# Kernel tuning notes

Hardware: AMD Instinct MI355X
Metric: run time of the kernel (lower is better)

Reference implementation:

```python
import jax, jax.numpy as jnp
import numpy as np

B, QS, FD = 16384, 1204, 7
N_CHUNKS, N_OFFSETS, WIN = 120, 5, 10


def setup_inputs() -> dict:
    key = jax.random.key(0)
    ks = jax.random.split(key, 10)
    s = 0.05
    return {
        "x": jax.random.normal(ks[0], (B, QS, FD), dtype=jnp.float32),
        "w_step": jax.random.normal(ks[1], (FD,), dtype=jnp.float32) * s,
        "b_step": jax.random.normal(ks[2], (), dtype=jnp.float32) * s,
        "wA": jax.random.normal(ks[3], (600, 128), dtype=jnp.float32) * s,
        "bA": jax.random.normal(ks[4], (128,), dtype=jnp.float32) * s,
        "wB": jax.random.normal(ks[5], (128, 32), dtype=jnp.float32) * s,
        "bB": jax.random.normal(ks[6], (32,), dtype=jnp.float32) * s,
        "wC": jax.random.normal(ks[7], (32, 2), dtype=jnp.float32) * s,
        "bC": jax.random.normal(ks[8], (2,), dtype=jnp.float32) * s,
    }


def reference(x, w_step, b_step, wA, bA, wB, bB, wC, bC):
    # fc_step: (b, qs, 7) -> (b, qs)
    out = jnp.einsum('bqf,f->bq', x, w_step) + b_step
    # Windowed max: starts[i, o] = o + i*10, window of size 10.
    starts = jnp.arange(N_CHUNKS)[:, None] * WIN + jnp.arange(N_OFFSETS)[None, :]  # (120, 5)
    idx = starts[..., None] + jnp.arange(WIN)  # (120, 5, 10)
    pooled = out[:, idx].max(axis=-1)  # (b, 120, 5)
    cat = pooled.reshape(x.shape[0], N_CHUNKS * N_OFFSETS)  # (b, 600)
    h = jax.nn.relu(cat @ wA + bA)
    h = jax.nn.relu(h @ wB + bB)
    return h @ wC + bC
```

## Files before the change

### kernel.cpp

```cpp
#include <hip/hip_runtime.h>

#define NB      16384
#define QS      1204
#define FD      7
#define ROWF    (QS * FD)
#define NCH     120
#define NOFF    5
#define WINSZ   10
#define CATN    600
#define H1N     128
#define H2N     32
#define OUTN    2
#define G       4
#define NTHR    256

__global__ __launch_bounds__(NTHR) void fused_struct3(
    const float* __restrict__ x,
    const float* __restrict__ w_step,
    const float* __restrict__ b_step,
    const float* __restrict__ wA,
    const float* __restrict__ bA,
    const float* __restrict__ wB,
    const float* __restrict__ bB,
    const float* __restrict__ wC,
    const float* __restrict__ bC,
    float* __restrict__ out)
{
    __shared__ __align__(16) float orow_s[G][QS];
    __shared__ __align__(16) float cat_s[G][CATN];
    __shared__ __align__(16) float h1_s[G][H1N];
    __shared__ __align__(16) float h2_s[G][H2N];

    const int t    = threadIdx.x;
    const int lane = t & 63;
    const int w    = t >> 6;
    const int b0   = blockIdx.x * G;

    const float w0 = w_step[0], w1 = w_step[1], w2 = w_step[2], w3 = w_step[3],
                w4 = w_step[4], w5 = w_step[5], w6 = w_step[6];
    const float bs = b_step[0];

    {
        const float* row = x + (size_t)(b0 + w) * ROWF;
        for (int q = lane; q < QS; q += 64) {
            const float* p = row + q * FD;
            float s = fmaf(p[0], w0, bs);
            s = fmaf(p[1], w1, s);
            s = fmaf(p[2], w2, s);
            s = fmaf(p[3], w3, s);
            s = fmaf(p[4], w4, s);
            s = fmaf(p[5], w5, s);
            s = fmaf(p[6], w6, s);
            orow_s[w][q] = s;
        }
    }
    __syncthreads();

    for (int j = t; j < G * CATN; j += NTHR) {
        int g  = j / CATN;
        int jj = j - g * CATN;
        int ci = jj / NOFF;
        int o  = jj - ci * NOFF;
        int st = ci * WINSZ + o;
        float m = orow_s[g][st];
        #pragma unroll
        for (int u = 1; u < WINSZ; ++u) m = fmaxf(m, orow_s[g][st + u]);
        cat_s[g][jj] = m;
    }
    __syncthreads();

    float4* red = (float4*)&orow_s[0][0];
    {
        const int c4 = t & 31;
        const int g  = (t >> 5) & 3;
        const int kh = t >> 7;
        const int k0 = kh * (CATN / 2);
        const float* wAp = wA + (size_t)k0 * H1N + 4 * c4;
        const float* cp  = &cat_s[g][k0];
        float4 acc = make_float4(0.f, 0.f, 0.f, 0.f);
        #pragma unroll 4
        for (int k = 0; k < CATN / 2; ++k) {
            const float4 a = *(const float4*)(wAp + (size_t)k * H1N);
            const float  c = cp[k];
            acc.x = fmaf(c, a.x, acc.x);
            acc.y = fmaf(c, a.y, acc.y);
            acc.z = fmaf(c, a.z, acc.z);
            acc.w = fmaf(c, a.w, acc.w);
        }
        red[t] = acc;
    }
    __syncthreads();
    if (t < 128) {
        const int c4 = t & 31;
        const int g  = t >> 5;
        const float4 a = red[t];
        const float4 b = red[t + 128];
        const float4 bias = *(const float4*)(bA + 4 * c4);
        h1_s[g][4 * c4 + 0] = fmaxf(a.x + b.x + bias.x, 0.f);
        h1_s[g][4 * c4 + 1] = fmaxf(a.y + b.y + bias.y, 0.f);
        h1_s[g][4 * c4 + 2] = fmaxf(a.z + b.z + bias.z, 0.f);
        h1_s[g][4 * c4 + 3] = fmaxf(a.w + b.w + bias.w, 0.f);
    }
    __syncthreads();

    if (t < G * H2N) {
        const int g = t >> 5;
        const int n = t & 31;
        float acc = bB[n];
        #pragma unroll 8
        for (int k = 0; k < H1N; ++k)
            acc = fmaf(h1_s[g][k], wB[k * H2N + n], acc);
        h2_s[g][n] = fmaxf(acc, 0.f);
    }
    __syncthreads();

    if (t < G * OUTN) {
        const int g = t >> 1;
        const int c = t & 1;
        float acc = bC[c];
        #pragma unroll
        for (int k = 0; k < H2N; ++k)
            acc = fmaf(h2_s[g][k], wC[k * OUTN + c], acc);
        out[(size_t)(b0 + g) * OUTN + c] = acc;
    }
}

extern "C" void kernel_launch(void* const* d_in, const int* in_sizes, int n_in,
                              void* d_out, int out_size, void* d_ws, size_t ws_size,
                              hipStream_t stream) {
    const float* x      = (const float*)d_in[0];
    const float* w_step = (const float*)d_in[1];
    const float* b_step = (const float*)d_in[2];
    const float* wA     = (const float*)d_in[3];
    const float* bA     = (const float*)d_in[4];
    const float* wB     = (const float*)d_in[5];
    const float* bB     = (const float*)d_in[6];
    const float* wC     = (const float*)d_in[7];
    const float* bC     = (const float*)d_in[8];
    float* out = (float*)d_out;

    dim3 grid(NB / G);
    fused_struct3<<<grid, NTHR, 0, stream>>>(
        x, w_step, b_step, wA, bA, wB, bB, wC, bC, out);
}
```

Before: 852.8 us.

## Vectorize projection loads, share window prefix maxima, reuse wA across batch rows

The step projection now loads seven float4 per lane and produces four outputs at once, with the shared row padded so these vector stores stay in bounds. Pooling computes the five offset windows of a chunk from shared suffix and prefix maxima instead of five separate 10-element scans. The first dense layer splits K into eight slices, with each thread handling all four batch rows so every wA load is reused four times. The partial sums are then reduced across slices. A launch-bounds occupancy hint is also added, which trades more registers per thread against fewer global weight reads.

```diff
diff --git a/kernel.cpp b/kernel.cpp
--- a/kernel.cpp
+++ b/kernel.cpp
@@ -2,6 +2,7 @@
 
 #define NB      16384
 #define QS      1204
+#define QSP     1216
 #define FD      7
 #define ROWF    (QS * FD)
 #define NCH     120
@@ -14,7 +15,7 @@
 #define G       4
 #define NTHR    256
 
-__global__ __launch_bounds__(NTHR) void fused_struct3(
+__global__ __launch_bounds__(NTHR, 5) void fused_struct3(
     const float* __restrict__ x,
     const float* __restrict__ w_step,
     const float* __restrict__ b_step,
@@ -26,7 +27,7 @@
     const float* __restrict__ bC,
     float* __restrict__ out)
 {
-    __shared__ __align__(16) float orow_s[G][QS];
+    __shared__ __align__(16) float orow_s[G][QSP];
     __shared__ __align__(16) float cat_s[G][CATN];
     __shared__ __align__(16) float h1_s[G][H1N];
     __shared__ __align__(16) float h2_s[G][H2N];
@@ -42,64 +43,121 @@
 
     {
         const float* row = x + (size_t)(b0 + w) * ROWF;
-        for (int q = lane; q < QS; q += 64) {
-            const float* p = row + q * FD;
-            float s = fmaf(p[0], w0, bs);
-            s = fmaf(p[1], w1, s);
-            s = fmaf(p[2], w2, s);
-            s = fmaf(p[3], w3, s);
-            s = fmaf(p[4], w4, s);
-            s = fmaf(p[5], w5, s);
-            s = fmaf(p[6], w6, s);
-            orow_s[w][q] = s;
-        }
-    }
-    __syncthreads();
-
-    for (int j = t; j < G * CATN; j += NTHR) {
-        int g  = j / CATN;
-        int jj = j - g * CATN;
-        int ci = jj / NOFF;
-        int o  = jj - ci * NOFF;
-        int st = ci * WINSZ + o;
-        float m = orow_s[g][st];
+        for (int i = 0; i < 5; ++i) {
+            const int q0 = i * 256 + 4 * lane;
+            if (q0 < QS) {
+                const float4* p = (const float4*)(row + q0 * FD);
+                const float4 v0 = p[0], v1 = p[1], v2 = p[2], v3 = p[3],
+                             v4 = p[4], v5 = p[5], v6 = p[6];
+                float s0 = bs, s1 = bs, s2 = bs, s3 = bs;
+                s0 = fmaf(v0.x, w0, s0); s0 = fmaf(v0.y, w1, s0); s0 = fmaf(v0.z, w2, s0);
+                s0 = fmaf(v0.w, w3, s0); s0 = fmaf(v1.x, w4, s0); s0 = fmaf(v1.y, w5, s0);
+                s0 = fmaf(v1.z, w6, s0);
+                s1 = fmaf(v1.w, w0, s1); s1 = fmaf(v2.x, w1, s1); s1 = fmaf(v2.y, w2, s1);
+                s1 = fmaf(v2.z, w3, s1); s1 = fmaf(v2.w, w4, s1); s1 = fmaf(v3.x, w5, s1);
+                s1 = fmaf(v3.y, w6, s1);
+                s2 = fmaf(v3.z, w0, s2); s2 = fmaf(v3.w, w1, s2); s2 = fmaf(v4.x, w2, s2);
+                s2 = fmaf(v4.y, w3, s2); s2 = fmaf(v4.z, w4, s2); s2 = fmaf(v4.w, w5, s2);
+                s2 = fmaf(v5.x, w6, s2);
+                s3 = fmaf(v5.y, w0, s3); s3 = fmaf(v5.z, w1, s3); s3 = fmaf(v5.w, w2, s3);
+                s3 = fmaf(v6.x, w3, s3); s3 = fmaf(v6.y, w4, s3); s3 = fmaf(v6.z, w5, s3);
+                s3 = fmaf(v6.w, w6, s3);
+                *(float4*)&orow_s[w][q0] = make_float4(s0, s1, s2, s3);
+            }
+        }
+    }
+    __syncthreads();
+
+    #pragma unroll
+    for (int it = 0; it < 2; ++it) {
+        const int item = t + it * NTHR;
+        if (item < G * NCH) {
+            const int g  = item / NCH;
+            const int ci = item - g * NCH;
+            const float* v = &orow_s[g][ci * WINSZ];
+            const float4 a = *(const float4*)(v + 0);
+            const float4 b = *(const float4*)(v + 4);
+            const float4 c = *(const float4*)(v + 8);
+            const float4 d = *(const float4*)(v + 12);
+            float s9 = b.w + c.x - c.x;
+            s9 = c.y;
+            float s8 = fmaxf(c.x, s9);
+            float s7 = fmaxf(b.w, s8);
+            float s6 = fmaxf(b.z, s7);
+            float s5 = fmaxf(b.y, s6);
+            float s4 = fmaxf(b.x, s5);
+            float s3 = fmaxf(a.w, s4);
+            float s2 = fmaxf(a.z, s3);
+            float s1 = fmaxf(a.y, s2);
+            float s0 = fmaxf(a.x, s1);
+            const float p10 = c.z;
+            const float p11 = fmaxf(p10, c.w);
+            const float p12 = fmaxf(p11, d.x);
+            const float p13 = fmaxf(p12, d.y);
+            float* cp = &cat_s[g][ci * NOFF];
+            cp[0] = s0;
+            cp[1] = fmaxf(s1, p10);
+            cp[2] = fmaxf(s2, p11);
+            cp[3] = fmaxf(s3, p12);
+            cp[4] = fmaxf(s4, p13);
+        }
+    }
+    __syncthreads();
+
+    float4* red4 = (float4*)&orow_s[0][0];
+    {
+        const int c4  = t & 31;
+        const int kh  = t >> 5;
+        const int k0  = kh * 76;
+        const int len = (kh == 7) ? 68 : 76;
+        const float* wAp = wA + (size_t)k0 * H1N + 4 * c4;
+        float4 acc0 = make_float4(0.f, 0.f, 0.f, 0.f);
+        float4 acc1 = acc0, acc2 = acc0, acc3 = acc0;
+        for (int kb = 0; kb < len; kb += 4) {
+            const float4 c0 = *(const float4*)&cat_s[0][k0 + kb];
+            const float4 c1 = *(const float4*)&cat_s[1][k0 + kb];
+            const float4 c2 = *(const float4*)&cat_s[2][k0 + kb];
+            const float4 c3 = *(const float4*)&cat_s[3][k0 + kb];
+            #pragma unroll
+            for (int r = 0; r < 4; ++r) {
+                const float4 a = *(const float4*)(wAp + (size_t)(kb + r) * H1N);
+                const float e0 = (r == 0) ? c0.x : (r == 1) ? c0.y : (r == 2) ? c0.z : c0.w;
+                const float e1 = (r == 0) ? c1.x : (r == 1) ? c1.y : (r == 2) ? c1.z : c1.w;
+                const float e2 = (r == 0) ? c2.x : (r == 1) ? c2.y : (r == 2) ? c2.z : c2.w;
+                const float e3 = (r == 0) ? c3.x : (r == 1) ? c3.y : (r == 2) ? c3.z : c3.w;
+                acc0.x = fmaf(e0, a.x, acc0.x); acc0.y = fmaf(e0, a.y, acc0.y);
+                acc0.z = fmaf(e0, a.z, acc0.z); acc0.w = fmaf(e0, a.w, acc0.w);
+                acc1.x = fmaf(e1, a.x, acc1.x); acc1.y = fmaf(e1, a.y, acc1.y);
+                acc1.z = fmaf(e1, a.z, acc1.z); acc1.w = fmaf(e1, a.w, acc1.w);
+                acc2.x = fmaf(e2, a.x, acc2.x); acc2.y = fmaf(e2, a.y, acc2.y);
+                acc2.z = fmaf(e2, a.z, acc2.z); acc2.w = fmaf(e2, a.w, acc2.w);
+                acc3.x = fmaf(e3, a.x, acc3.x); acc3.y = fmaf(e3, a.y, acc3.y);
+                acc3.z = fmaf(e3, a.z, acc3.z); acc3.w = fmaf(e3, a.w, acc3.w);
+            }
+        }
+        const int base = (kh * 32 + c4) * 4;
+        red4[base + 0] = acc0;
+        red4[base + 1] = acc1;
+        red4[base + 2] = acc2;
+        red4[base + 3] = acc3;
+    }
+    __syncthreads();
+    if (t < 128) {
+        const int c4r = t >> 2;
+        const int g   = t & 3;
+        float4 s = red4[(0 * 32 + c4r) * 4 + g];
         #pragma unroll
-        for (int u = 1; u < WINSZ; ++u) m = fmaxf(m, orow_s[g][st + u]);
-        cat_s[g][jj] = m;
-    }
-    __syncthreads();
-
-    float4* red = (float4*)&orow_s[0][0];
-    {
-        const int c4 = t & 31;
-        const int g  = (t >> 5) & 3;
-        const int kh = t >> 7;
-        const int k0 = kh * (CATN / 2);
-        const float* wAp = wA + (size_t)k0 * H1N + 4 * c4;
-        const float* cp  = &cat_s[g][k0];
-        float4 acc = make_float4(0.f, 0.f, 0.f, 0.f);
-        #pragma unroll 4
-        for (int k = 0; k < CATN / 2; ++k) {
-            const float4 a = *(const float4*)(wAp + (size_t)k * H1N);
-            const float  c = cp[k];
-            acc.x = fmaf(c, a.x, acc.x);
-            acc.y = fmaf(c, a.y, acc.y);
-            acc.z = fmaf(c, a.z, acc.z);
-            acc.w = fmaf(c, a.w, acc.w);
-        }
-        red[t] = acc;
-    }
-    __syncthreads();
-    if (t < 128) {
-        const int c4 = t & 31;
-        const int g  = t >> 5;
-        const float4 a = red[t];
-        const float4 b = red[t + 128];
-        const float4 bias = *(const float4*)(bA + 4 * c4);
-        h1_s[g][4 * c4 + 0] = fmaxf(a.x + b.x + bias.x, 0.f);
-        h1_s[g][4 * c4 + 1] = fmaxf(a.y + b.y + bias.y, 0.f);
-        h1_s[g][4 * c4 + 2] = fmaxf(a.z + b.z + bias.z, 0.f);
-        h1_s[g][4 * c4 + 3] = fmaxf(a.w + b.w + bias.w, 0.f);
+        for (int kh = 1; kh < 8; ++kh) {
+            const float4 r = red4[(kh * 32 + c4r) * 4 + g];
+            s.x += r.x; s.y += r.y; s.z += r.z; s.w += r.w;
+        }
+        const float4 bias = *(const float4*)(bA + 4 * c4r);
+        float4 h;
+        h.x = fmaxf(s.x + bias.x, 0.f);
+        h.y = fmaxf(s.y + bias.y, 0.f);
+        h.z = fmaxf(s.z + bias.z, 0.f);
+        h.w = fmaxf(s.w + bias.w, 0.f);
+        *(float4*)&h1_s[g][4 * c4r] = h;
     }
     __syncthreads();
 
```

Result: faster. 763.4 us (-10.5%).
